# Optimization experiments

Hardware: AMD Instinct MI355X
Metric: run time of the kernel (lower is better)

Reference implementation:

```python
import jax, jax.numpy as jnp
import numpy as np


def setup_inputs() -> dict:
    key = jax.random.key(0)
    kq, kk, kv, kl = jax.random.split(key, 4)
    B, Nq, Nkv, D = 16, 2048, 2048, 64
    return {
        "Q_batch": jax.random.normal(kq, (B, Nq, D), dtype=jnp.float32),
        "K_batch": jax.random.normal(kk, (B, Nkv, D), dtype=jnp.float32),
        "V_batch": jax.random.normal(kv, (B, Nkv, D), dtype=jnp.float32),
        "valid_lens": jax.random.randint(kl, (B,), 0, Nkv, dtype=jnp.int64 if jax.config.jax_enable_x64 else jnp.int32),
    }


def reference(Q_batch, K_batch, V_batch, valid_lens):
    # S: (B, Nq, Nkv) scaled dot-product scores
    d = Q_batch.shape[-1]
    scale = 1.0 / jnp.sqrt(jnp.asarray(d, Q_batch.dtype))
    S = jnp.einsum('bqd,bkd->bqk', Q_batch, K_batch) * scale
    # mask_first_n_valid: position k valid iff k < valid_lens[b], broadcast over queries
    kv_idx = jnp.arange(S.shape[-1])  # (Nkv,)
    mask = kv_idx[None, None, :] < valid_lens[:, None, None]  # (B, 1->Nq, Nkv)
    S = jnp.where(mask, S, jnp.asarray(-1e20, S.dtype))
    W = jax.nn.softmax(S, axis=-1)  # attention weights (dropout rate = 0.0)
    return jnp.einsum('bqk,bkv->bqv', W, V_batch)
```

## Files before the change

### kernel.cpp

```cpp
#include <hip/hip_runtime.h>

#define BATCH 16
#define NQ    2048
#define NKV   2048
#define DH    64
#define SC    0.18033688011112042f
#define TILE_B 8192

typedef __attribute__((ext_vector_type(8))) short  bf16x8;
typedef __attribute__((ext_vector_type(4))) unsigned u32x4;
typedef __attribute__((ext_vector_type(16))) float f32x16;

__device__ __forceinline__ unsigned f2bf(float f) {
  unsigned u = __builtin_bit_cast(unsigned, f);
  u += 0x7FFFu + ((u >> 16) & 1u);
  return u >> 16;
}

__global__ __launch_bounds__(256) void convert_kernel(
    const float* __restrict__ K, const float* __restrict__ V,
    const int* __restrict__ lens, unsigned char* __restrict__ WS) {
  const int bt = blockIdx.x;
  const int b = bt >> 6, t = bt & 63;
  const int L = lens[b];
  const int Leff = (L == 0) ? NKV : L;
  if (t * 32 >= Leff) return;

  unsigned char* tile = WS + (size_t)bt * TILE_B;
  const size_t   srow = ((size_t)b * NKV + (size_t)t * 32) * DH;
  const int tid = threadIdx.x;
  const int l = tid & 63, g = tid >> 6;
  const int l31 = l & 31, hi = l >> 5;
  {
    const float4* p = (const float4*)(K + srow + (size_t)l31 * DH + g * 16 + hi * 8);
    float4 a = p[0], c4 = p[1];
    bf16x8 w;
    w[0] = (short)f2bf(a.x);  w[1] = (short)f2bf(a.y);
    w[2] = (short)f2bf(a.z);  w[3] = (short)f2bf(a.w);
    w[4] = (short)f2bf(c4.x); w[5] = (short)f2bf(c4.y);
    w[6] = (short)f2bf(c4.z); w[7] = (short)f2bf(c4.w);
    *(bf16x8*)(tile + g * 1024 + l * 16) = w;
  }
  {
    const int c2 = g & 1, dh = g >> 1;
    const float* vp = V + srow + (size_t)(c2 * 16 + 4 * hi) * DH + dh * 32 + l31;
    bf16x8 w;
#pragma unroll
    for (int j = 0; j < 8; ++j)
      w[j] = (short)f2bf(vp[(size_t)((j & 3) + 8 * (j >> 2)) * DH]);
    *(bf16x8*)(tile + 4096 + g * 1024 + l * 16) = w;
  }
}

__global__ __launch_bounds__(256, 3) void sdpa_kernel(
    const float* __restrict__ Q, const unsigned char* __restrict__ WS,
    const int* __restrict__ lens, float* __restrict__ O) {
  __shared__ float smem[6336];

  const int tid  = threadIdx.x;
  const int lane = tid & 63;
  const int wave = tid >> 6;
  const int l31  = lane & 31, hi = lane >> 5;

  const int idx = blockIdx.x, layer = idx >> 8, rr = idx & 255;
  const int b   = (rr + layer * 3) & 15;
  const int qo  = (rr >> 4) + layer * 16;

  const int  L    = lens[b];
  const bool zlen = (L == 0);
  const int  Leff = zlen ? NKV : L;
  const int  nT   = (Leff + 31) >> 5;
  const int  tb   = (nT * wave) >> 2;
  const int  cnt  = ((nT * (wave + 1)) >> 2) - tb;
  const int  tmask = (!zlen && (L & 31)) ? nT - 1 : -1;

  bf16x8 Qf[4];
  {
    const float sc = zlen ? 0.f : SC;
    const float* qp = Q + ((size_t)b * NQ + qo * 32 + l31) * DH + hi * 8;
#pragma unroll
    for (int c = 0; c < 4; ++c) {
      const float4* p = (const float4*)(qp + c * 16);
      float4 a = p[0], d4 = p[1];
      bf16x8 w;
      w[0] = (short)f2bf(a.x * sc);  w[1] = (short)f2bf(a.y * sc);
      w[2] = (short)f2bf(a.z * sc);  w[3] = (short)f2bf(a.w * sc);
      w[4] = (short)f2bf(d4.x * sc); w[5] = (short)f2bf(d4.y * sc);
      w[6] = (short)f2bf(d4.z * sc); w[7] = (short)f2bf(d4.w * sc);
      Qf[c] = w;
    }
  }

  const unsigned char* gp = WS + (size_t)(b * 64 + tb) * TILE_B + lane * 16;

  f32x16 oc0, oc1;
  float  l_ = 0.f;
#pragma unroll
  for (int r = 0; r < 16; ++r) { oc0[r] = 0.f; oc1[r] = 0.f; }

  bf16x8 cur[8];
  if (cnt > 0) {
#pragma unroll
    for (int i = 0; i < 8; ++i) cur[i] = *(const bf16x8*)(gp + i * 1024);
  }

#pragma unroll 2
  for (int it = 0; it < cnt; ++it) {
    const int t = tb + it;
    const unsigned char* gn = (it + 1 < cnt) ? (gp + TILE_B) : gp;
    bf16x8 nxt[8];
#pragma unroll
    for (int i = 0; i < 8; ++i) nxt[i] = *(const bf16x8*)(gn + i * 1024);
    gp += TILE_B;

    f32x16 acc;
#pragma unroll
    for (int r = 0; r < 16; ++r) acc[r] = 0.f;
#pragma unroll
    for (int c = 0; c < 4; ++c)
      acc = __builtin_amdgcn_mfma_f32_32x32x16_bf16(cur[c], Qf[c], acc, 0, 0, 0);

    if (t == tmask) {
#pragma unroll
      for (int r = 0; r < 16; ++r) {
        const int key = t * 32 + (r & 3) + 8 * (r >> 2) + 4 * hi;
        if (key >= L) acc[r] = -1e30f;
      }
    }

    unsigned pi[16];
    float ls = 0.f;
#pragma unroll
    for (int r = 0; r < 16; ++r) {
      float p = __builtin_amdgcn_exp2f(acc[r]);
      ls += p;
      pi[r] = __builtin_bit_cast(unsigned, p) + 0x8000u;
    }
    l_ += ls;

    u32x4 t0, t1;
#pragma unroll
    for (int w = 0; w < 4; ++w) {
      t0[w] = __builtin_amdgcn_perm(pi[2 * w + 1], pi[2 * w], 0x07060302u);
      t1[w] = __builtin_amdgcn_perm(pi[8 + 2 * w + 1], pi[8 + 2 * w], 0x07060302u);
    }
    bf16x8 Pf0 = __builtin_bit_cast(bf16x8, t0);
    bf16x8 Pf1 = __builtin_bit_cast(bf16x8, t1);

    oc0 = __builtin_amdgcn_mfma_f32_32x32x16_bf16(cur[4], Pf0, oc0, 0, 0, 0);
    oc0 = __builtin_amdgcn_mfma_f32_32x32x16_bf16(cur[5], Pf1, oc0, 0, 0, 0);
    oc1 = __builtin_amdgcn_mfma_f32_32x32x16_bf16(cur[6], Pf0, oc1, 0, 0, 0);
    oc1 = __builtin_amdgcn_mfma_f32_32x32x16_bf16(cur[7], Pf1, oc1, 0, 0, 0);

#pragma unroll
    for (int i = 0; i < 8; ++i) cur[i] = nxt[i];
  }

  if (wave >= 1) {
    float* Mb = smem + (wave - 1) * 2112 + lane;
#pragma unroll
    for (int r = 0; r < 16; ++r) { Mb[r * 64] = oc0[r]; Mb[(16 + r) * 64] = oc1[r]; }
    Mb[32 * 64] = l_;
  }
  __syncthreads();
  if (wave == 0) {
#pragma unroll
    for (int w = 0; w < 3; ++w) {
      const float* Mb = smem + w * 2112 + lane;
#pragma unroll
      for (int r = 0; r < 16; ++r) { oc0[r] += Mb[r * 64]; oc1[r] += Mb[(16 + r) * 64]; }
      l_ += Mb[32 * 64];
    }
    const float inv = 1.0f / (l_ + __shfl_xor(l_, 32, 64));
#pragma unroll
    for (int r = 0; r < 16; ++r) {
      const int d0 = (r & 3) + 8 * (r >> 2) + 4 * hi;
      smem[l31 * 68 + d0]      = oc0[r] * inv;
      smem[l31 * 68 + 32 + d0] = oc1[r] * inv;
    }
  }
  __syncthreads();

  float* Ob = O + ((size_t)b * NQ + (size_t)qo * 32) * DH;
#pragma unroll
  for (int R = 0; R < 2; ++R) {
    const int fi = R * 256 + tid;
    const int q = fi >> 4, ch = fi & 15;
    float4 v4 = *(const float4*)&smem[q * 68 + ch * 4];
    *(float4*)(Ob + (size_t)q * DH + ch * 4) = v4;
  }
}

extern "C" void kernel_launch(void* const* d_in, const int* in_sizes, int n_in,
                              void* d_out, int out_size, void* d_ws, size_t ws_size,
                              hipStream_t stream) {
  const float* Q    = (const float*)d_in[0];
  const float* K    = (const float*)d_in[1];
  const float* V    = (const float*)d_in[2];
  const int*   lens = (const int*)d_in[3];
  float*       Out  = (float*)d_out;
  unsigned char* WS = (unsigned char*)d_ws;

  hipLaunchKernelGGL(convert_kernel, dim3(BATCH * 64), dim3(256), 0, stream, K, V, lens, WS);
  hipLaunchKernelGGL(sdpa_kernel, dim3(1024), dim3(256), 0, stream, Q, WS, lens, Out);
}
```

Measured before the change: 99.41 us.

## Balance work across blocks with stream-K split over query tiles and partial reduction

Replaces the fixed one-block-per-query-tile mapping with a stream-K style partition. The total KV-tile work, weighted by each batch's valid length plus a per-item overhead, is split evenly across 1024 blocks. Query tiles that span several blocks write partial O and l sums to a workspace, and the last block to arrive, detected with an atomic counter, reduces and stores them. This targets load imbalance from varying valid_lens, at the cost of extra global traffic, fences and atomics, and a counter reset in the convert kernel.

```diff
diff --git a/kernel.cpp b/kernel.cpp
--- a/kernel.cpp
+++ b/kernel.cpp
@@ -6,6 +6,10 @@
 #define DH    64
 #define SC    0.18033688011112042f
 #define TILE_B 8192
+#define EP     4
+#define GBLK   1024
+#define PART_OFF 8388608u
+#define CNT_OFF  146800640u
 
 typedef __attribute__((ext_vector_type(8))) short  bf16x8;
 typedef __attribute__((ext_vector_type(4))) unsigned u32x4;
@@ -21,6 +25,7 @@
     const float* __restrict__ K, const float* __restrict__ V,
     const int* __restrict__ lens, unsigned char* __restrict__ WS) {
   const int bt = blockIdx.x;
+  if (threadIdx.x == 0) ((int*)(WS + CNT_OFF))[bt] = 0;
   const int b = bt >> 6, t = bt & 63;
   const int L = lens[b];
   const int Leff = (L == 0) ? NKV : L;
@@ -53,141 +58,230 @@
 }
 
 __global__ __launch_bounds__(256, 3) void sdpa_kernel(
-    const float* __restrict__ Q, const unsigned char* __restrict__ WS,
+    const float* __restrict__ Q, unsigned char* __restrict__ WS,
     const int* __restrict__ lens, float* __restrict__ O) {
-  __shared__ float smem[6336];
+  __shared__ float smem[3 * 2112];
+  __shared__ int   sflag;
 
   const int tid  = threadIdx.x;
   const int lane = tid & 63;
   const int wave = tid >> 6;
   const int l31  = lane & 31, hi = lane >> 5;
-
-  const int idx = blockIdx.x, layer = idx >> 8, rr = idx & 255;
-  const int b   = (rr + layer * 3) & 15;
-  const int qo  = (rr >> 4) + layer * 16;
-
-  const int  L    = lens[b];
-  const bool zlen = (L == 0);
-  const int  Leff = zlen ? NKV : L;
-  const int  nT   = (Leff + 31) >> 5;
-  const int  tb   = (nT * wave) >> 2;
-  const int  cnt  = ((nT * (wave + 1)) >> 2) - tb;
-  const int  tmask = (!zlen && (L & 31)) ? nT - 1 : -1;
-
-  bf16x8 Qf[4];
-  {
-    const float sc = zlen ? 0.f : SC;
-    const float* qp = Q + ((size_t)b * NQ + qo * 32 + l31) * DH + hi * 8;
-#pragma unroll
-    for (int c = 0; c < 4; ++c) {
-      const float4* p = (const float4*)(qp + c * 16);
-      float4 a = p[0], d4 = p[1];
-      bf16x8 w;
-      w[0] = (short)f2bf(a.x * sc);  w[1] = (short)f2bf(a.y * sc);
-      w[2] = (short)f2bf(a.z * sc);  w[3] = (short)f2bf(a.w * sc);
-      w[4] = (short)f2bf(d4.x * sc); w[5] = (short)f2bf(d4.y * sc);
-      w[6] = (short)f2bf(d4.z * sc); w[7] = (short)f2bf(d4.w * sc);
-      Qf[c] = w;
+  const int idx  = blockIdx.x;
+
+  long long W = 0;
+#pragma unroll
+  for (int bb = 0; bb < 16; ++bb) {
+    const int L = lens[bb];
+    const int Leff = (L == 0) ? NKV : L;
+    W += 64ll * (((Leff + 31) >> 5) + EP);
+  }
+  const long long s = (long long)idx * W / GBLK;
+  const long long e = (long long)(idx + 1) * W / GBLK;
+
+  long long cum = 0;
+  int b = 0, nT = 0, cb = 0;
+  for (;;) {
+    const int L = lens[b];
+    const int Leff = (L == 0) ? NKV : L;
+    nT = (Leff + 31) >> 5;
+    cb = nT + EP;
+    const long long nb = 64ll * cb;
+    if (cum + nb > s) break;
+    cum += nb;
+    ++b;
+  }
+  int       item   = (int)((s - cum) / cb);
+  long long istart = cum + (long long)item * cb;
+  int       u0     = (int)(s - istart);
+
+  float* PART = (float*)(WS + PART_OFF);
+  int*   CNT  = (int*)(WS + CNT_OFF);
+
+  while (istart < e) {
+    const int  L    = lens[b];
+    const bool zlen = (L == 0);
+    const int  t0   = (u0 < nT) ? u0 : nT;
+    const long long rem = e - istart;
+    const int  t1   = (rem < (long long)nT) ? (int)rem : nT;
+
+    if (t0 < t1) {
+      const int qo    = item;
+      const int tmask = (!zlen && (L & 31)) ? nT - 1 : -1;
+      const int len   = t1 - t0;
+      const int wt0   = t0 + ((len * wave) >> 2);
+      const int cnt   = t0 + ((len * (wave + 1)) >> 2) - wt0;
+
+      bf16x8 Qf[4];
+      {
+        const float  sc = zlen ? 0.f : SC;
+        const float* qp = Q + ((size_t)b * NQ + qo * 32 + l31) * DH + hi * 8;
+#pragma unroll
+        for (int c = 0; c < 4; ++c) {
+          const float4* p = (const float4*)(qp + c * 16);
+          float4 a = p[0], d4 = p[1];
+          bf16x8 w;
+          w[0] = (short)f2bf(a.x * sc);  w[1] = (short)f2bf(a.y * sc);
+          w[2] = (short)f2bf(a.z * sc);  w[3] = (short)f2bf(a.w * sc);
+          w[4] = (short)f2bf(d4.x * sc); w[5] = (short)f2bf(d4.y * sc);
+          w[6] = (short)f2bf(d4.z * sc); w[7] = (short)f2bf(d4.w * sc);
+          Qf[c] = w;
+        }
+      }
+
+      f32x16 oc0, oc1;
+      float  l_ = 0.f;
+#pragma unroll
+      for (int r = 0; r < 16; ++r) { oc0[r] = 0.f; oc1[r] = 0.f; }
+
+      const unsigned char* gp = WS + (size_t)(b * 64 + wt0) * TILE_B + (size_t)lane * 16;
+      bf16x8 cur[8];
+      if (cnt > 0) {
+#pragma unroll
+        for (int i = 0; i < 8; ++i) cur[i] = *(const bf16x8*)(gp + i * 1024);
+      }
+
+#pragma unroll 2
+      for (int it = 0; it < cnt; ++it) {
+        const int t = wt0 + it;
+        const unsigned char* gn = (it + 1 < cnt) ? (gp + TILE_B) : gp;
+        bf16x8 nxt[8];
+#pragma unroll
+        for (int i = 0; i < 8; ++i) nxt[i] = *(const bf16x8*)(gn + i * 1024);
+        gp += TILE_B;
+
+        f32x16 acc;
+#pragma unroll
+        for (int r = 0; r < 16; ++r) acc[r] = 0.f;
+#pragma unroll
+        for (int c = 0; c < 4; ++c)
+          acc = __builtin_amdgcn_mfma_f32_32x32x16_bf16(cur[c], Qf[c], acc, 0, 0, 0);
+
+        if (t == tmask) {
+#pragma unroll
+          for (int r = 0; r < 16; ++r) {
+            const int key = t * 32 + (r & 3) + 8 * (r >> 2) + 4 * hi;
+            if (key >= L) acc[r] = -1e30f;
+          }
+        }
+
+        unsigned pi[16];
+        float ls = 0.f;
+#pragma unroll
+        for (int r = 0; r < 16; ++r) {
+          float p = __builtin_amdgcn_exp2f(acc[r]);
+          ls += p;
+          pi[r] = __builtin_bit_cast(unsigned, p) + 0x8000u;
+        }
+        l_ += ls;
+
+        u32x4 t0v, t1v;
+#pragma unroll
+        for (int w = 0; w < 4; ++w) {
+          t0v[w] = __builtin_amdgcn_perm(pi[2 * w + 1], pi[2 * w], 0x07060302u);
+          t1v[w] = __builtin_amdgcn_perm(pi[8 + 2 * w + 1], pi[8 + 2 * w], 0x07060302u);
+        }
+        bf16x8 Pf0 = __builtin_bit_cast(bf16x8, t0v);
+        bf16x8 Pf1 = __builtin_bit_cast(bf16x8, t1v);
+
+        oc0 = __builtin_amdgcn_mfma_f32_32x32x16_bf16(cur[4], Pf0, oc0, 0, 0, 0);
+        oc0 = __builtin_amdgcn_mfma_f32_32x32x16_bf16(cur[5], Pf1, oc0, 0, 0, 0);
+        oc1 = __builtin_amdgcn_mfma_f32_32x32x16_bf16(cur[6], Pf0, oc1, 0, 0, 0);
+        oc1 = __builtin_amdgcn_mfma_f32_32x32x16_bf16(cur[7], Pf1, oc1, 0, 0, 0);
+
+#pragma unroll
+        for (int i = 0; i < 8; ++i) cur[i] = nxt[i];
+      }
+
+      __syncthreads();
+      if (wave >= 1) {
+        float* Mb = smem + (wave - 1) * 2112 + lane;
+#pragma unroll
+        for (int r = 0; r < 16; ++r) { Mb[r * 64] = oc0[r]; Mb[(16 + r) * 64] = oc1[r]; }
+        Mb[32 * 64] = l_;
+      }
+      __syncthreads();
+      if (wave == 0) {
+#pragma unroll
+        for (int w = 0; w < 3; ++w) {
+          const float* Mb = smem + w * 2112 + lane;
+#pragma unroll
+          for (int r = 0; r < 16; ++r) { oc0[r] += Mb[r * 64]; oc1[r] += Mb[(16 + r) * 64]; }
+          l_ += Mb[32 * 64];
+        }
+#pragma unroll
+        for (int r = 0; r < 16; ++r) {
+          smem[r * 64 + lane]        = oc0[r];
+          smem[(16 + r) * 64 + lane] = oc1[r];
+        }
+        smem[32 * 64 + lane] = l_;
+      }
+      __syncthreads();
+
+      const int f0    = (int)(((istart + 1) * GBLK - 1) / W);
+      const int f1    = (int)(((istart + nT) * GBLK - 1) / W);
+      const int npart = f1 - f0 + 1;
+      bool doStore = true;
+      const int qid = b * 64 + qo;
+      if (npart > 1) {
+        const int j = idx - f0;
+        float* dst = PART + (size_t)(qid * 16 + j) * 2112;
+#pragma unroll
+        for (int k = 0; k < 9; ++k) {
+          const int ii = k * 256 + tid;
+          if (ii < 2112) dst[ii] = smem[ii];
+        }
+        __threadfence();
+        __syncthreads();
+        if (tid == 0) sflag = atomicAdd(&CNT[qid], 1);
+        __syncthreads();
+        if (sflag != npart - 1) {
+          doStore = false;
+        } else {
+          __threadfence();
+          for (int jj = 0; jj < npart; ++jj) {
+            if (jj == idx - f0) continue;
+            const float* src = PART + (size_t)(qid * 16 + jj) * 2112;
+#pragma unroll
+            for (int k = 0; k < 9; ++k) {
+              const int ii = k * 256 + tid;
+              if (ii < 2112) smem[ii] += src[ii];
+            }
+          }
+          __syncthreads();
+        }
+      }
+
+      if (doStore) {
+        const int   q   = tid >> 3, db = (tid & 7) * 8;
+        const float lq  = smem[32 * 64 + q] + smem[32 * 64 + 32 + q];
+        const float inv = 1.0f / lq;
+        float out[8];
+#pragma unroll
+        for (int dd = 0; dd < 8; ++dd) {
+          const int d = db + dd, dh = d >> 5, d5 = d & 31;
+          const int h2 = (d5 >> 2) & 1, r = (d5 & 3) | ((d5 >> 3) << 2);
+          out[dd] = smem[(dh * 16 + r) * 64 + h2 * 32 + q] * inv;
+        }
+        float* Ob = O + ((size_t)b * NQ + qo * 32 + q) * DH + db;
+        *(float4*)Ob       = (float4){out[0], out[1], out[2], out[3]};
+        *(float4*)(Ob + 4) = (float4){out[4], out[5], out[6], out[7]};
+      }
     }
-  }
-
-  const unsigned char* gp = WS + (size_t)(b * 64 + tb) * TILE_B + lane * 16;
-
-  f32x16 oc0, oc1;
-  float  l_ = 0.f;
-#pragma unroll
-  for (int r = 0; r < 16; ++r) { oc0[r] = 0.f; oc1[r] = 0.f; }
-
-  bf16x8 cur[8];
-  if (cnt > 0) {
-#pragma unroll
-    for (int i = 0; i < 8; ++i) cur[i] = *(const bf16x8*)(gp + i * 1024);
-  }
-
-#pragma unroll 2
-  for (int it = 0; it < cnt; ++it) {
-    const int t = tb + it;
-    const unsigned char* gn = (it + 1 < cnt) ? (gp + TILE_B) : gp;
-    bf16x8 nxt[8];
-#pragma unroll
-    for (int i = 0; i < 8; ++i) nxt[i] = *(const bf16x8*)(gn + i * 1024);
-    gp += TILE_B;
-
-    f32x16 acc;
-#pragma unroll
-    for (int r = 0; r < 16; ++r) acc[r] = 0.f;
-#pragma unroll
-    for (int c = 0; c < 4; ++c)
-      acc = __builtin_amdgcn_mfma_f32_32x32x16_bf16(cur[c], Qf[c], acc, 0, 0, 0);
-
-    if (t == tmask) {
-#pragma unroll
-      for (int r = 0; r < 16; ++r) {
-        const int key = t * 32 + (r & 3) + 8 * (r >> 2) + 4 * hi;
-        if (key >= L) acc[r] = -1e30f;
+
+    istart += cb;
+    ++item;
+    u0 = 0;
+    if (item >= 64) {
+      ++b;
+      item = 0;
+      if (b < BATCH) {
+        const int L2 = lens[b];
+        const int Le = (L2 == 0) ? NKV : L2;
+        nT = (Le + 31) >> 5;
+        cb = nT + EP;
       }
     }
-
-    unsigned pi[16];
-    float ls = 0.f;
-#pragma unroll
-    for (int r = 0; r < 16; ++r) {
-      float p = __builtin_amdgcn_exp2f(acc[r]);
-      ls += p;
-      pi[r] = __builtin_bit_cast(unsigned, p) + 0x8000u;
-    }
-    l_ += ls;
-
-    u32x4 t0, t1;
-#pragma unroll
-    for (int w = 0; w < 4; ++w) {
-      t0[w] = __builtin_amdgcn_perm(pi[2 * w + 1], pi[2 * w], 0x07060302u);
-      t1[w] = __builtin_amdgcn_perm(pi[8 + 2 * w + 1], pi[8 + 2 * w], 0x07060302u);
-    }
-    bf16x8 Pf0 = __builtin_bit_cast(bf16x8, t0);
-    bf16x8 Pf1 = __builtin_bit_cast(bf16x8, t1);
-
-    oc0 = __builtin_amdgcn_mfma_f32_32x32x16_bf16(cur[4], Pf0, oc0, 0, 0, 0);
-    oc0 = __builtin_amdgcn_mfma_f32_32x32x16_bf16(cur[5], Pf1, oc0, 0, 0, 0);
-    oc1 = __builtin_amdgcn_mfma_f32_32x32x16_bf16(cur[6], Pf0, oc1, 0, 0, 0);
-    oc1 = __builtin_amdgcn_mfma_f32_32x32x16_bf16(cur[7], Pf1, oc1, 0, 0, 0);
-
-#pragma unroll
-    for (int i = 0; i < 8; ++i) cur[i] = nxt[i];
-  }
-
-  if (wave >= 1) {
-    float* Mb = smem + (wave - 1) * 2112 + lane;
-#pragma unroll
-    for (int r = 0; r < 16; ++r) { Mb[r * 64] = oc0[r]; Mb[(16 + r) * 64] = oc1[r]; }
-    Mb[32 * 64] = l_;
-  }
-  __syncthreads();
-  if (wave == 0) {
-#pragma unroll
-    for (int w = 0; w < 3; ++w) {
-      const float* Mb = smem + w * 2112 + lane;
-#pragma unroll
-      for (int r = 0; r < 16; ++r) { oc0[r] += Mb[r * 64]; oc1[r] += Mb[(16 + r) * 64]; }
-      l_ += Mb[32 * 64];
-    }
-    const float inv = 1.0f / (l_ + __shfl_xor(l_, 32, 64));
-#pragma unroll
-    for (int r = 0; r < 16; ++r) {
-      const int d0 = (r & 3) + 8 * (r >> 2) + 4 * hi;
-      smem[l31 * 68 + d0]      = oc0[r] * inv;
-      smem[l31 * 68 + 32 + d0] = oc1[r] * inv;
-    }
-  }
-  __syncthreads();
-
-  float* Ob = O + ((size_t)b * NQ + (size_t)qo * 32) * DH;
-#pragma unroll
-  for (int R = 0; R < 2; ++R) {
-    const int fi = R * 256 + tid;
-    const int q = fi >> 4, ch = fi & 15;
-    float4 v4 = *(const float4*)&smem[q * 68 + ch * 4];
-    *(float4*)(Ob + (size_t)q * DH + ch * 4) = v4;
   }
 }
 
@@ -202,5 +296,5 @@
   unsigned char* WS = (unsigned char*)d_ws;
 
   hipLaunchKernelGGL(convert_kernel, dim3(BATCH * 64), dim3(256), 0, stream, K, V, lens, WS);
-  hipLaunchKernelGGL(sdpa_kernel, dim3(1024), dim3(256), 0, stream, Q, WS, lens, Out);
+  hipLaunchKernelGGL(sdpa_kernel, dim3(GBLK), dim3(256), 0, stream, Q, WS, lens, Out);
 }
```

Measured after the change: 367.8 us. 3.7x slower.
